# Performance work log

Hardware: AMD Instinct MI355X
Metric: run time of the kernel (lower is better)

Reference implementation:

```python
import jax, jax.numpy as jnp
import numpy as np
from jax import lax

SD = 16          # sample_duration
STRIDE = 16      # feat_stride
SCALES = (4, 8, 16)
RATIOS = (0.5, 1.0, 2.0)
PRE_NMS = 1000   # proposals kept before NMS (TEST config)
POST_NMS = 128   # proposals kept after NMS
NMS_TH = 0.7


def _anchors2d():
    base = 16.0
    ctr = (base - 1.0) / 2.0
    out = []
    for r in RATIOS:
        ws = np.round(np.sqrt(base * base / r))
        hs = np.round(ws * r)
        for s in SCALES:
            w, h = ws * s, hs * s
            out.append([ctr - (w - 1) / 2, ctr - (h - 1) / 2,
                        ctr + (w - 1) / 2, ctr + (h - 1) / 2])
    return np.asarray(out, np.float32)                       # (9, 4)


def _anchors3d():
    # tube anchors: (x1, y1, t1, x2, y2, t2), durations [SD, SD/2, SD/4]
    a2 = _anchors2d()
    out = []
    for d in (SD, SD // 2, SD // 4):
        for a in a2:
            out.append([a[0], a[1], 0.0, a[2], a[3], d - 1.0])
    return np.asarray(out, np.float32)                       # (27, 6)


def _shifted(anchors, H, W):
    k = anchors.shape[-1]
    sx = jnp.arange(W, dtype=jnp.float32) * STRIDE
    sy = jnp.arange(H, dtype=jnp.float32) * STRIDE
    if k == 4:
        sh = jnp.stack(jnp.broadcast_arrays(sx[None, :], sy[:, None],
                                            sx[None, :], sy[:, None]), -1)
    else:
        z = jnp.zeros((H, W), jnp.float32)
        sh = jnp.stack(jnp.broadcast_arrays(sx[None, :], sy[:, None], z,
                                            sx[None, :], sy[:, None], z), -1)
    return (sh[:, :, None, :] + jnp.asarray(anchors)[None, None]).reshape(-1, k)


def _decode(anchors, deltas):
    # deltas layout: (d_ctr..., d_logsize...); works for 2D (k=4) and 3D (k=6)
    nd = anchors.shape[-1] // 2
    lo, hi = anchors[..., :nd], anchors[..., nd:]
    size = hi - lo + 1.0
    ctr = lo + 0.5 * (size - 1.0)
    pctr = deltas[..., :nd] * size + ctr
    psize = jnp.exp(deltas[..., nd:]) * size
    return jnp.concatenate([pctr - 0.5 * (psize - 1.0),
                            pctr + 0.5 * (psize - 1.0)], -1)


def _iou(b, boxes):
    # b: (k,), boxes: (N, k); area/volume IoU with +1 pixel convention
    nd = boxes.shape[-1] // 2
    lo = jnp.maximum(b[:nd], boxes[:, :nd])
    hi = jnp.minimum(b[nd:], boxes[:, nd:])
    inter = jnp.prod(jnp.maximum(hi - lo + 1.0, 0.0), -1)
    va = jnp.prod(b[nd:] - b[:nd] + 1.0)
    vb = jnp.prod(boxes[:, nd:] - boxes[:, :nd] + 1.0, -1)
    return inter / (va + vb - inter)


def _nms(boxes):
    # boxes already sorted by descending score; greedy NMS, fixed output size
    N = boxes.shape[0]

    def body(i, c):
        supp, keep = c
        idx = jnp.argmax(~supp)                 # first unsuppressed box
        keep = keep.at[i].set(idx.astype(jnp.int32))
        supp = supp | (_iou(boxes[idx], boxes) > NMS_TH)
        supp = supp.at[idx].set(True)
        return supp, keep

    _, keep = lax.fori_loop(0, POST_NMS, body,
                            (jnp.zeros(N, bool), jnp.zeros(POST_NMS, jnp.int32)))
    return keep


def _proposals(scores, deltas, anchors, maxs):
    # scores (B,N), deltas (B,N,k), anchors (N,k), maxs (B,1,k)
    boxes = jnp.clip(_decode(anchors[None], deltas), 0.0, maxs)
    _, idx = lax.top_k(scores, PRE_NMS)
    bx = jnp.take_along_axis(boxes, idx[..., None], axis=1)   # (B,PRE,k)
    keep = jax.vmap(_nms)(bx)                                 # (B,POST)
    sel = jnp.take_along_axis(bx, keep[..., None], axis=1)    # (B,POST,k)
    bidx = jnp.broadcast_to(
        jnp.arange(sel.shape[0], dtype=sel.dtype)[:, None, None],
        sel.shape[:2] + (1,))
    return lax.stop_gradient(jnp.concatenate([bidx, sel], -1))


def setup_inputs() -> dict:
    k = jax.random.split(jax.random.key(0), 8)
    s = 0.01
    return {
        "base_feat": jax.random.normal(k[0], (1, 256, 16, 32, 32), jnp.float32),
        "im_info": jnp.array([[512.0, 512.0, 1.0]], jnp.float32),
        "gt_boxes": jax.random.uniform(k[1], (1, 5, 7), jnp.float32) * 100.0,
        "gt_rois": jax.random.uniform(k[2], (1, 5, 16, 5), jnp.float32) * 100.0,
        "W_conv": jax.random.normal(k[3], (512, 256, 3, 3, 3), jnp.float32) * s,
        "b_conv": jnp.zeros((512,), jnp.float32),
        "W_cls": jax.random.normal(k[4], (54, 512), jnp.float32) * s,
        "b_cls": jnp.zeros((54,), jnp.float32),
        "W_bbox": jax.random.normal(k[5], (162, 512), jnp.float32) * s,
        "b_bbox": jnp.zeros((162,), jnp.float32),
        "W_cls16": jax.random.normal(k[6], (18, 512), jnp.float32) * s,
        "b_cls16": jnp.zeros((18,), jnp.float32),
        "W_bbox16": jax.random.normal(k[7], (36, 512), jnp.float32) * s,
        "b_bbox16": jnp.zeros((36,), jnp.float32),
    }


def reference(base_feat, im_info, gt_boxes, gt_rois, W_conv, b_conv,
              W_cls, b_cls, W_bbox, b_bbox, W_cls16, b_cls16,
              W_bbox16, b_bbox16):
    B, _, T, H, W = base_feat.shape
    # RPN_Conv: 3x3x3 Conv3d + ReLU
    conv1 = jax.nn.relu(
        lax.conv_general_dilated(base_feat, W_conv, (1, 1, 1), "SAME",
                                 dimension_numbers=("NCDHW", "OIDHW", "NCDHW"))
        + b_conv[None, :, None, None, None])
    # 1x1x1 score / bbox heads (3D)
    cls3 = jnp.einsum("bcthw,oc->bothw", conv1, W_cls) + b_cls[None, :, None, None, None]
    bbox3 = jnp.einsum("bcthw,oc->bothw", conv1, W_bbox) + b_bbox[None, :, None, None, None]
    # permute(0,1,3,4,2).mean(4) == mean over the temporal axis
    feat2 = conv1.mean(axis=2)
    cls2 = jnp.einsum("bchw,oc->bohw", feat2, W_cls16) + b_cls16[None, :, None, None]
    bbox2 = jnp.einsum("bchw,oc->bohw", feat2, W_bbox16) + b_bbox16[None, :, None, None]
    # reshape(x,2) + softmax over dim 1; fg prob is the second half of channels
    fg3 = jax.nn.softmax(cls3.reshape(B, 2, 27, T, H, W), axis=1)[:, 1]  # (B,27,T,H,W)
    fg2 = jax.nn.softmax(cls2.reshape(B, 2, 9, H, W), axis=1)[:, 1]      # (B,9,H,W)
    # proposal layers consume detached tensors (torch .data)
    fg3, fg2, bbox3d, bbox2d = map(lax.stop_gradient, (fg3, fg2, bbox3, bbox2))
    # flatten position-major (h, w, anchor)
    sc3 = fg3.mean(axis=2).transpose(0, 2, 3, 1).reshape(B, -1)
    dl3 = bbox3d.mean(axis=2).reshape(B, 27, 6, H, W).transpose(0, 3, 4, 1, 2).reshape(B, -1, 6)
    sc2 = fg2.transpose(0, 2, 3, 1).reshape(B, -1)
    dl2 = bbox2d.reshape(B, 9, 4, H, W).transpose(0, 3, 4, 1, 2).reshape(B, -1, 4)
    imh, imw = im_info[:, 0][:, None], im_info[:, 1][:, None]
    sdm = jnp.full_like(imw, SD - 1.0)
    max3 = jnp.stack([imw - 1, imh - 1, sdm, imw - 1, imh - 1, sdm], -1)  # (B,1,6)
    max2 = jnp.stack([imw - 1, imh - 1, imw - 1, imh - 1], -1)            # (B,1,4)
    rois = _proposals(sc3, dl3, _shifted(_anchors3d(), H, W), max3)       # (B,POST,7)
    rois16 = _proposals(sc2, dl2, _shifted(_anchors2d(), H, W), max2)     # (B,POST,5)
    z = jnp.zeros((), jnp.float32)  # eval mode: all RPN losses are 0
    return rois, rois16, z, z, z, z
```

## Files before the change

kernel.cpp:

```cpp
#include <hip/hip_runtime.h>
#include <hip/hip_bf16.h>
#include <cfloat>
#include <cstdint>


#define T_DIM 16
#define H_DIM 32
#define W_DIM 32
#define NVOX  (T_DIM*H_DIM*W_DIM)
#define HW    (H_DIM*W_DIM)
#define CIN   256
#define COUT  512
#define PRE_NMS 1000
#define POST_NMS 128
#define NMS_TH 0.7f

typedef __attribute__((ext_vector_type(8))) short v8s;
typedef __attribute__((ext_vector_type(4))) float v4f;
typedef __attribute__((ext_vector_type(4))) int v4i;

#define MFMA_B16(A,B,C) __builtin_amdgcn_mfma_f32_16x16x32_bf16(A,B,C,0,0,0)

__device__ __forceinline__ short f2bf(float x) {
    unsigned u = __float_as_uint(x);
    u += 0x7FFFu + ((u >> 16) & 1u);
    return (short)(u >> 16);
}
__device__ __forceinline__ float bf2f(short s) {
    return __uint_as_float(((unsigned)(unsigned short)s) << 16);
}
__device__ __forceinline__ int pk(short a, short b) {
    return (int)((unsigned short)a | ((unsigned)(unsigned short)b << 16));
}

__constant__ float c_ws[3] = {23.f, 16.f, 11.f};
__constant__ float c_hs[3] = {12.f, 16.f, 22.f};
__constant__ float c_sc[3] = {4.f, 8.f, 16.f};
__constant__ float c_depth[3] = {16.f, 8.f, 4.f};

__global__ void k_split_w(const float* __restrict__ W, short* __restrict__ A0,
                          short* __restrict__ A1, short* __restrict__ A2) {
    int i = blockIdx.x * 256 + threadIdx.x;
    int c7 = i & 7;
    int o = (i >> 3) & 511;
    int ko = (i >> 12) & 31;
    int tap = i >> 17;
    int c = ko * 8 + c7;
    float x = W[(o * 256 + c) * 27 + tap];
    short h = f2bf(x); float r = x - bf2f(h);
    short m = f2bf(r); float r2 = r - bf2f(m);
    short l = f2bf(r2);
    A0[i] = h; A1[i] = m; A2[i] = l;
}

__global__ void k_build_wcomb(const float* __restrict__ Wcls, const float* __restrict__ Wbb,
                              float* __restrict__ Wc) {
    int i = blockIdx.x * 256 + threadIdx.x;
    int o = i & 255;
    int c = i >> 8;
    float v = 0.f;
    if (o < 54) v = Wcls[o * 512 + c];
    else if (o < 216) v = Wbb[(o - 54) * 512 + c];
    Wc[i] = v;
}

#define SP8(X0,X1,X2,X3,X4,X5,X6,X7, OH, OM, OL) {                            \
    short h0_=f2bf(X0), h1_=f2bf(X1), h2_=f2bf(X2), h3_=f2bf(X3);             \
    short h4_=f2bf(X4), h5_=f2bf(X5), h6_=f2bf(X6), h7_=f2bf(X7);             \
    float r0_=(X0)-bf2f(h0_), r1_=(X1)-bf2f(h1_), r2_=(X2)-bf2f(h2_);         \
    float r3_=(X3)-bf2f(h3_), r4_=(X4)-bf2f(h4_), r5_=(X5)-bf2f(h5_);         \
    float r6_=(X6)-bf2f(h6_), r7_=(X7)-bf2f(h7_);                             \
    short m0_=f2bf(r0_), m1_=f2bf(r1_), m2_=f2bf(r2_), m3_=f2bf(r3_);         \
    short m4_=f2bf(r4_), m5_=f2bf(r5_), m6_=f2bf(r6_), m7_=f2bf(r7_);         \
    short l0_=f2bf(r0_-bf2f(m0_)), l1_=f2bf(r1_-bf2f(m1_));                   \
    short l2_=f2bf(r2_-bf2f(m2_)), l3_=f2bf(r3_-bf2f(m3_));                   \
    short l4_=f2bf(r4_-bf2f(m4_)), l5_=f2bf(r5_-bf2f(m5_));                   \
    short l6_=f2bf(r6_-bf2f(m6_)), l7_=f2bf(r7_-bf2f(m7_));                   \
    OH = (v4i){pk(h0_,h1_), pk(h2_,h3_), pk(h4_,h5_), pk(h6_,h7_)};           \
    OM = (v4i){pk(m0_,m1_), pk(m2_,m3_), pk(m4_,m5_), pk(m6_,m7_)};           \
    OL = (v4i){pk(l0_,l1_), pk(l2_,l3_), pk(l4_,l5_), pk(l6_,l7_)};           \
}

#define CV_SHIFT(TAP) {                                                       \
    int kt_ = (TAP) / 9 - 1, kh_ = ((TAP) / 3) % 3 - 1, kw_ = (TAP) % 3 - 1;  \
    int tt_ = bt + kt_, hh_ = bh + kh_, ww_ = bw + kw_;                       \
    bVal = ((unsigned)tt_ < 16u) && ((unsigned)hh_ < 32u) && ((unsigned)ww_ < 32u); \
    bOff = bVal ? ((tt_ << 10) + (hh_ << 5) + ww_) : 0;                       \
}

#define CV_LOAD_B(CK) {                                                       \
    const float* ip_ = I + ((size_t)((CK) + skh * 16) << 14) + bOff;          \
    float x0_  = bVal ? ip_[0]        : 0.f;                                  \
    float x1_  = bVal ? ip_[1 << 14]  : 0.f;                                  \
    float x2_  = bVal ? ip_[2 << 14]  : 0.f;                                  \
    float x3_  = bVal ? ip_[3 << 14]  : 0.f;                                  \
    float x4_  = bVal ? ip_[4 << 14]  : 0.f;                                  \
    float x5_  = bVal ? ip_[5 << 14]  : 0.f;                                  \
    float x6_  = bVal ? ip_[6 << 14]  : 0.f;                                  \
    float x7_  = bVal ? ip_[7 << 14]  : 0.f;                                  \
    float x8_  = bVal ? ip_[8 << 14]  : 0.f;                                  \
    float x9_  = bVal ? ip_[9 << 14]  : 0.f;                                  \
    float x10_ = bVal ? ip_[10 << 14] : 0.f;                                  \
    float x11_ = bVal ? ip_[11 << 14] : 0.f;                                  \
    float x12_ = bVal ? ip_[12 << 14] : 0.f;                                  \
    float x13_ = bVal ? ip_[13 << 14] : 0.f;                                  \
    float x14_ = bVal ? ip_[14 << 14] : 0.f;                                  \
    float x15_ = bVal ? ip_[15 << 14] : 0.f;                                  \
    SP8(x0_,x1_,x2_,x3_,x4_,x5_,x6_,x7_,       pbh0, pbm0, pbl0);             \
    SP8(x8_,x9_,x10_,x11_,x12_,x13_,x14_,x15_, pbh1, pbm1, pbl1);             \
}

__global__ __launch_bounds__(256) void k_conv3d_mfma(
        const float* __restrict__ I, const short* __restrict__ A0,
        const short* __restrict__ A1, const short* __restrict__ A2,
        const float* __restrict__ bias, float* __restrict__ O) {
    __shared__ v4i Bsh[3][512];
    const int tid = threadIdx.x;
    const int o0 = blockIdx.y * 128;
    const int v0 = blockIdx.x * 128;
    const int lane = tid & 63;
    const int wv = tid >> 6;
    const int quad = lane >> 4, m16 = lane & 15;
    const int wo = (wv >> 1) * 64;
    const int wvx = (wv & 1) * 64;

    const int sa_o = tid >> 1, skh = tid & 1;
    const int uW0 = (skh * 2) * 128 + sa_o;
    const int uW1 = (skh * 2 + 1) * 128 + sa_o;

    const int vbase = v0 + sa_o;
    const int bt = vbase >> 10, bh = (vbase >> 5) & 31, bw = vbase & 31;

    const int uB = quad * 128 + wvx + m16;

    const size_t aLane = ((size_t)(o0 + wo + m16) << 3) + ((size_t)quad << 12);

    v4f acc[4][4];
#pragma unroll
    for (int i = 0; i < 4; i++)
#pragma unroll
        for (int j = 0; j < 4; j++) acc[i][j] = (v4f){0.f, 0.f, 0.f, 0.f};

    int bOff, bVal;
    v4i pbh0, pbh1, pbm0, pbm1, pbl0, pbl1;

    CV_SHIFT(0);
    CV_LOAD_B(0);

    for (int s = 0; s < 216; ++s) {
        __syncthreads();
        Bsh[0][uW0] = pbh0; Bsh[0][uW1] = pbh1;
        Bsh[1][uW0] = pbm0; Bsh[1][uW1] = pbm1;
        Bsh[2][uW0] = pbl0; Bsh[2][uW1] = pbl1;
        __syncthreads();
        const int tap = s >> 3;
        const size_t aBase = (((size_t)tap * 32 + ((s & 7) << 2)) << 12) + aLane;
        v8s ah0 = *(const v8s*)(A0 + aBase);
        v8s ah1 = *(const v8s*)(A0 + aBase + 16 * 8);
        v8s ah2 = *(const v8s*)(A0 + aBase + 32 * 8);
        v8s ah3 = *(const v8s*)(A0 + aBase + 48 * 8);
        v8s am0 = *(const v8s*)(A1 + aBase);
        v8s am1 = *(const v8s*)(A1 + aBase + 16 * 8);
        v8s am2 = *(const v8s*)(A1 + aBase + 32 * 8);
        v8s am3 = *(const v8s*)(A1 + aBase + 48 * 8);
        v8s al0 = *(const v8s*)(A2 + aBase);
        v8s al1 = *(const v8s*)(A2 + aBase + 16 * 8);
        v8s al2 = *(const v8s*)(A2 + aBase + 32 * 8);
        v8s al3 = *(const v8s*)(A2 + aBase + 48 * 8);
        {
            int s1 = s + 1;
            if (s1 < 216) {
                int tap1 = s1 >> 3, ck1 = (s1 & 7) << 5;
                if ((s1 & 7) == 0) CV_SHIFT(tap1);
                CV_LOAD_B(ck1);
            }
        }
#pragma unroll
        for (int j = 0; j < 4; ++j) {
            v8s bb = *(const v8s*)(&Bsh[0][uB + j * 16]);
            v8s bm = *(const v8s*)(&Bsh[1][uB + j * 16]);
            v8s bl = *(const v8s*)(&Bsh[2][uB + j * 16]);
            v4f a;
            a = acc[0][j];
            a = MFMA_B16(ah0, bb, a); a = MFMA_B16(ah0, bm, a);
            a = MFMA_B16(am0, bb, a); a = MFMA_B16(ah0, bl, a);
            a = MFMA_B16(am0, bm, a); a = MFMA_B16(al0, bb, a);
            acc[0][j] = a;
            a = acc[1][j];
            a = MFMA_B16(ah1, bb, a); a = MFMA_B16(ah1, bm, a);
            a = MFMA_B16(am1, bb, a); a = MFMA_B16(ah1, bl, a);
            a = MFMA_B16(am1, bm, a); a = MFMA_B16(al1, bb, a);
            acc[1][j] = a;
            a = acc[2][j];
            a = MFMA_B16(ah2, bb, a); a = MFMA_B16(ah2, bm, a);
            a = MFMA_B16(am2, bb, a); a = MFMA_B16(ah2, bl, a);
            a = MFMA_B16(am2, bm, a); a = MFMA_B16(al2, bb, a);
            acc[2][j] = a;
            a = acc[3][j];
            a = MFMA_B16(ah3, bb, a); a = MFMA_B16(ah3, bm, a);
            a = MFMA_B16(am3, bb, a); a = MFMA_B16(ah3, bl, a);
            a = MFMA_B16(am3, bm, a); a = MFMA_B16(al3, bb, a);
            acc[3][j] = a;
        }
    }

#pragma unroll
    for (int i = 0; i < 4; ++i) {
#pragma unroll
        for (int r = 0; r < 4; ++r) {
            int o = o0 + wo + i * 16 + quad * 4 + r;
            float bo = bias[o];
            float* dst = O + (size_t)o * NVOX + v0 + wvx + m16;
#pragma unroll
            for (int j = 0; j < 4; ++j)
                dst[j * 16] = fmaxf(acc[i][j][r] + bo, 0.f);
        }
    }
}

__global__ __launch_bounds__(256) void k_gemm_logits3(const float* __restrict__ conv1,
                                                      const float* __restrict__ Wc,
                                                      float* __restrict__ L) {
    __shared__ float As[16][128];
    __shared__ float Bs[16][128];
    const int tid = threadIdx.x;
    const int o0 = blockIdx.y * 128;
    const int v0 = blockIdx.x * 128;
    const int ty = tid >> 4, tx = tid & 15;

    float acc[8][8];
#pragma unroll
    for (int i = 0; i < 8; i++)
#pragma unroll
        for (int j = 0; j < 8; j++) acc[i][j] = 0.f;

    for (int ck = 0; ck < 512; ck += 16) {
        __syncthreads();
#pragma unroll
        for (int r = 0; r < 2; ++r) {
            int f = tid + r * 256;
            int c_l = f >> 5, o4 = (f & 31) << 2;
            *(float4*)(&As[c_l][o4]) = *(const float4*)(Wc + ((size_t)(ck + c_l) << 8) + o0 + o4);
        }
#pragma unroll
        for (int r = 0; r < 2; ++r) {
            int f = tid + r * 256;
            int c_l = f >> 5, v4 = (f & 31) << 2;
            *(float4*)(&Bs[c_l][v4]) = *(const float4*)(conv1 + ((size_t)(ck + c_l) << 14) + v0 + v4);
        }
        __syncthreads();
#pragma unroll
        for (int k = 0; k < 16; ++k) {
            float a[8], b[8];
            *(float4*)(a)     = *(const float4*)(&As[k][ty * 4]);
            *(float4*)(a + 4) = *(const float4*)(&As[k][64 + ty * 4]);
            *(float4*)(b)     = *(const float4*)(&Bs[k][tx * 4]);
            *(float4*)(b + 4) = *(const float4*)(&Bs[k][64 + tx * 4]);
#pragma unroll
            for (int i = 0; i < 8; i++)
#pragma unroll
                for (int j = 0; j < 8; j++)
                    acc[i][j] = fmaf(a[i], b[j], acc[i][j]);
        }
    }
#pragma unroll
    for (int i = 0; i < 8; i++) {
        int orow = (i < 4) ? (ty * 4 + i) : (64 + ty * 4 + (i - 4));
        float* dst = L + (size_t)(o0 + orow) * NVOX + v0;
        *(float4*)(dst + tx * 4)      = *(const float4*)(&acc[i][0]);
        *(float4*)(dst + 64 + tx * 4) = *(const float4*)(&acc[i][4]);
    }
}

__global__ void k_sc3(const float* __restrict__ L, const float* __restrict__ b_cls,
                      float* __restrict__ sc3) {
    int i = blockIdx.x * 256 + threadIdx.x;
    if (i >= 27 * HW) return;
    int a = i >> 10, hw = i & 1023;
    float b0 = b_cls[a], b1 = b_cls[27 + a];
    const float* L0 = L + (size_t)a * NVOX + hw;
    const float* L1 = L + (size_t)(27 + a) * NVOX + hw;
    float s = 0.f;
    for (int t = 0; t < T_DIM; t++) {
        float x0 = L0[t * HW] + b0, x1 = L1[t * HW] + b1;
        float m = fmaxf(x0, x1);
        float e0 = expf(x0 - m), e1 = expf(x1 - m);
        s += e1 / (e0 + e1);
    }
    sc3[hw * 27 + a] = s * (1.f / 16.f);
}

__global__ void k_dl3(const float* __restrict__ L, const float* __restrict__ b_bbox,
                      float* __restrict__ dl3) {
    int i = blockIdx.x * 256 + threadIdx.x;
    if (i >= 162 * HW) return;
    int ch = i >> 10, hw = i & 1023;
    const float* Lr = L + (size_t)(54 + ch) * NVOX + hw;
    float s = 0.f;
    for (int t = 0; t < T_DIM; t++) s += Lr[t * HW];
    s = s * (1.f / 16.f) + b_bbox[ch];
    int a = ch / 6, d = ch - a * 6;
    dl3[((size_t)hw * 27 + a) * 6 + d] = s;
}

__global__ void k_feat2(const float* __restrict__ conv1, float* __restrict__ feat2) {
    int i = blockIdx.x * 256 + threadIdx.x;
    int c = i >> 10, hw = i & 1023;
    const float* src = conv1 + (size_t)c * NVOX + hw;
    float s = 0.f;
    for (int t = 0; t < T_DIM; t++) s += src[t * HW];
    feat2[i] = s * (1.f / 16.f);
}

__global__ void k_gemm2d(const float* __restrict__ feat2, const float* __restrict__ Wcls16,
                         const float* __restrict__ Wbb16, float* __restrict__ L2) {
    int g = blockIdx.x * 256 + threadIdx.x;
    int o = g >> 10, hw = g & 1023;
    const float* wrow = (o < 18) ? (Wcls16 + (size_t)o * 512) : (Wbb16 + (size_t)(o - 18) * 512);
    float s = 0.f;
    for (int c = 0; c < 512; c++) s = fmaf(wrow[c], feat2[(size_t)c * HW + hw], s);
    L2[(size_t)o * HW + hw] = s;
}

__global__ void k_sc2(const float* __restrict__ L2, const float* __restrict__ b_cls16,
                      float* __restrict__ sc2) {
    int i = blockIdx.x * 256 + threadIdx.x;
    if (i >= 9 * HW) return;
    int a = i >> 10, hw = i & 1023;
    float x0 = L2[(size_t)a * HW + hw] + b_cls16[a];
    float x1 = L2[(size_t)(9 + a) * HW + hw] + b_cls16[9 + a];
    float m = fmaxf(x0, x1);
    float e0 = expf(x0 - m), e1 = expf(x1 - m);
    sc2[hw * 9 + a] = e1 / (e0 + e1);
}

__global__ void k_dl2(const float* __restrict__ L2, const float* __restrict__ b_bbox16,
                      float* __restrict__ dl2) {
    int i = blockIdx.x * 256 + threadIdx.x;
    if (i >= 36 * HW) return;
    int ch = i >> 10, hw = i & 1023;
    float v = L2[(size_t)(18 + ch) * HW + hw] + b_bbox16[ch];
    int a = ch >> 2, d = ch & 3;
    dl2[((size_t)hw * 9 + a) * 4 + d] = v;
}

__device__ __forceinline__ unsigned mapf(float f) {
    unsigned u = __float_as_uint(f);
    return (u & 0x80000000u) ? ~u : (u | 0x80000000u);
}

__global__ __launch_bounds__(1024) void k_proposal(const float* __restrict__ im_info,
                                                   const float* __restrict__ sc3,
                                                   const float* __restrict__ dl3,
                                                   const float* __restrict__ sc2,
                                                   const float* __restrict__ dl2,
                                                   float* __restrict__ out) {
    const int branch = blockIdx.x;
    const int tid = threadIdx.x;
    const int A = (branch == 0) ? 27 : 9;
    const int nd = (branch == 0) ? 3 : 2;
    const float* scores = (branch == 0) ? sc3 : sc2;
    const float* deltas = (branch == 0) ? dl3 : dl2;
    const int K = PRE_NMS;
    const int ept = A;
    const int base = tid * ept;

    __shared__ unsigned hist[256];
    __shared__ unsigned long long keys[1024];
    __shared__ float bx[PRE_NMS][6];
    __shared__ int keep[POST_NMS];
    __shared__ unsigned wsum[16];
    __shared__ unsigned long long alive[16];
    __shared__ int sh_b, sh_next, bcast;

    unsigned prefix = 0;
    int rank = K;
    for (int shift = 24; shift >= 0; shift -= 8) {
        if (tid < 256) hist[tid] = 0;
        __syncthreads();
        const unsigned mask_hi = (shift == 24) ? 0u : (0xFFFFFFFFu << (shift + 8));
        for (int j = 0; j < ept; j++) {
            unsigned m = mapf(scores[base + j]);
            if ((m & mask_hi) == prefix)
                atomicAdd(&hist[(m >> shift) & 255], 1u);
        }
        __syncthreads();
        for (int d = 1; d < 256; d <<= 1) {
            unsigned add = 0;
            if (tid < 256 && tid + d < 256) add = hist[tid + d];
            __syncthreads();
            if (tid < 256) hist[tid] += add;
            __syncthreads();
        }
        if (tid < 256) {
            bool win = (hist[tid] >= (unsigned)rank) &&
                       (tid == 255 || hist[tid + 1] < (unsigned)rank);
            if (win) { sh_b = tid; sh_next = (tid == 255) ? 0 : (int)hist[tid + 1]; }
        }
        __syncthreads();
        prefix |= (unsigned)sh_b << shift;
        rank -= sh_next;
        __syncthreads();
    }
    const unsigned tau = prefix;

    int gt_c = 0, eq_c = 0;
    for (int j = 0; j < ept; j++) {
        unsigned m = mapf(scores[base + j]);
        gt_c += (m > tau);
        eq_c += (m == tau);
    }
    unsigned cnt = ((unsigned)gt_c << 16) | (unsigned)eq_c;
    const int lane = tid & 63, wid = tid >> 6;
    unsigned x = cnt;
    for (int d = 1; d < 64; d <<= 1) {
        unsigned y = __shfl_up(x, d);
        if (lane >= d) x += y;
    }
    if (lane == 63) wsum[wid] = x;
    __syncthreads();
    if (wid == 0) {
        unsigned w = (lane < 16) ? wsum[lane] : 0;
        for (int d = 1; d < 16; d <<= 1) {
            unsigned y = __shfl_up(w, d);
            if (lane >= d) w += y;
        }
        if (lane < 16) wsum[lane] = w;
    }
    __syncthreads();
    unsigned excl = x - cnt + (wid ? wsum[wid - 1] : 0);
    const int c1 = (int)(wsum[15] >> 16);
    int gi = (int)(excl >> 16);
    int ei = (int)(excl & 0xFFFFu);
    for (int j = 0; j < ept; j++) {
        int idx = base + j;
        unsigned m = mapf(scores[idx]);
        unsigned long long key = ((unsigned long long)m << 32) |
                                 (unsigned)(0xFFFFFFFFu - (unsigned)idx);
        if (m > tau) {
            keys[gi++] = key;
        } else if (m == tau) {
            if (c1 + ei < K) keys[c1 + ei] = key;
            ei++;
        }
    }
    if (tid < 1024 - K) keys[K + tid] = 0;
    __syncthreads();

    for (int k = 2; k <= 1024; k <<= 1) {
        for (int j = k >> 1; j > 0; j >>= 1) {
            int ixj = tid ^ j;
            if (ixj > tid) {
                unsigned long long a = keys[tid], b = keys[ixj];
                bool sw2 = ((tid & k) == 0) ? (a < b) : (a > b);
                if (sw2) { keys[tid] = b; keys[ixj] = a; }
            }
            __syncthreads();
        }
    }

    const float imh = im_info[0], imw = im_info[1];
    if (tid < K) {
        int n = (int)(0xFFFFFFFFu - (unsigned)(keys[tid] & 0xFFFFFFFFull));
        int cell = n / A, a = n - cell * A;
        int hc = cell >> 5, wc = cell & 31;
        int a2 = (branch == 0) ? (a % 9) : a;
        int ri = a2 / 3, si = a2 % 3;
        float w = c_ws[ri] * c_sc[si], h = c_hs[ri] * c_sc[si];
        float lo[3], hi[3], mx[3];
        lo[0] = 7.5f - (w - 1.f) * 0.5f + 16.f * wc;
        hi[0] = 7.5f + (w - 1.f) * 0.5f + 16.f * wc;
        mx[0] = imw - 1.f;
        lo[1] = 7.5f - (h - 1.f) * 0.5f + 16.f * hc;
        hi[1] = 7.5f + (h - 1.f) * 0.5f + 16.f * hc;
        mx[1] = imh - 1.f;
        if (branch == 0) { lo[2] = 0.f; hi[2] = c_depth[a / 9] - 1.f; mx[2] = (float)(T_DIM - 1); }
        const float* dp = deltas + (size_t)n * (2 * nd);
        for (int d = 0; d < nd; d++) {
            float size = hi[d] - lo[d] + 1.f;
            float ctr = lo[d] + 0.5f * (size - 1.f);
            float pctr = dp[d] * size + ctr;
            float psize = expf(dp[nd + d]) * size;
            float pl = pctr - 0.5f * (psize - 1.f);
            float ph = pctr + 0.5f * (psize - 1.f);
            bx[tid][d]      = fminf(fmaxf(pl, 0.f), mx[d]);
            bx[tid][nd + d] = fminf(fmaxf(ph, 0.f), mx[d]);
        }
    }
    if (tid < 16) alive[tid] = (tid < 15) ? ~0ull : ((1ull << (K - 15 * 64)) - 1);
    __syncthreads();

    float myb[6]; float myvol = 1.f;
    if (tid < K) {
        for (int d = 0; d < 6; d++) myb[d] = bx[tid][d];
        for (int d = 0; d < nd; d++) myvol *= (myb[nd + d] - myb[d] + 1.f);
    }
    for (int i = 0; i < POST_NMS; ++i) {
        if (tid < 64) {
            unsigned long long wvb = (tid < 16) ? alive[tid] : 0ull;
            int cand = wvb ? (tid * 64 + __ffsll(wvb) - 1) : 0x7fffffff;
#pragma unroll
            for (int off = 32; off; off >>= 1)
                cand = min(cand, __shfl_xor(cand, off));
            if (tid == 0) {
                int m = (cand == 0x7fffffff) ? 0 : cand;
                bcast = m; keep[i] = m;
            }
        }
        __syncthreads();
        int sel = bcast;
        bool s = false;
        if (tid < K) {
            float inter = 1.f, selvol = 1.f;
            for (int d = 0; d < nd; d++) {
                float slo = bx[sel][d], shi = bx[sel][nd + d];
                float l = fmaxf(slo, myb[d]);
                float hh = fminf(shi, myb[nd + d]);
                inter *= fmaxf(hh - l + 1.f, 0.f);
                selvol *= (shi - slo + 1.f);
            }
            float iou = inter / (selvol + myvol - inter);
            s = (iou > NMS_TH) || (tid == sel);
        }
        unsigned long long bal = __ballot(s);
        if (lane == 0 && bal) alive[wid] &= ~bal;
        __syncthreads();
    }

    if (tid < POST_NMS) {
        int k = keep[tid];
        if (branch == 0) {
            float* o = out + (size_t)tid * 7;
            o[0] = 0.f;
            for (int d = 0; d < 6; d++) o[1 + d] = bx[k][d];
        } else {
            float* o = out + 128 * 7 + (size_t)tid * 5;
            o[0] = 0.f;
            for (int d = 0; d < 4; d++) o[1 + d] = bx[k][d];
        }
    }
    if (branch == 0 && tid == 0) {
        out[1536] = 0.f; out[1537] = 0.f; out[1538] = 0.f; out[1539] = 0.f;
    }
}

extern "C" void kernel_launch(void* const* d_in, const int* in_sizes, int n_in,
                              void* d_out, int out_size, void* d_ws, size_t ws_size,
                              hipStream_t stream) {
    (void)in_sizes; (void)n_in; (void)out_size; (void)ws_size;
    const float* base_feat = (const float*)d_in[0];
    const float* im_info   = (const float*)d_in[1];
    const float* W_conv    = (const float*)d_in[4];
    const float* b_conv    = (const float*)d_in[5];
    const float* W_cls     = (const float*)d_in[6];
    const float* b_cls     = (const float*)d_in[7];
    const float* W_bbox    = (const float*)d_in[8];
    const float* b_bbox    = (const float*)d_in[9];
    const float* W_cls16   = (const float*)d_in[10];
    const float* b_cls16   = (const float*)d_in[11];
    const float* W_bbox16  = (const float*)d_in[12];
    const float* b_bbox16  = (const float*)d_in[13];
    float* out = (float*)d_out;

    char* ws = (char*)d_ws;
    const size_t AW = (size_t)27 * 512 * 256;
    short* A0 = (short*)ws;
    short* A1 = A0 + AW;
    short* A2 = A1 + AW;
    float* L3 = (float*)ws;
    size_t off = AW * 3 * sizeof(short);
    float* Wcomb  = (float*)(ws + off); off += (size_t)512 * 256 * 4;
    float* conv1  = (float*)(ws + off); off += (size_t)COUT * NVOX * 4;
    float* feat2  = (float*)(ws + off); off += (size_t)512 * HW * 4;
    float* L2     = (float*)(ws + off); off += (size_t)64 * HW * 4;
    float* sc3    = (float*)(ws + off); off += (size_t)27 * HW * 4;
    float* dl3    = (float*)(ws + off); off += (size_t)27 * HW * 6 * 4;
    float* sc2    = (float*)(ws + off); off += (size_t)9 * HW * 4;
    float* dl2    = (float*)(ws + off); off += (size_t)9 * HW * 4 * 4;

    k_split_w<<<13824, 256, 0, stream>>>(W_conv, A0, A1, A2);
    k_build_wcomb<<<512, 256, 0, stream>>>(W_cls, W_bbox, Wcomb);
    {
        dim3 g(NVOX / 128, COUT / 128);
        k_conv3d_mfma<<<g, 256, 0, stream>>>(base_feat, A0, A1, A2, b_conv, conv1);
    }
    {
        dim3 g(NVOX / 128, 2);
        k_gemm_logits3<<<g, 256, 0, stream>>>(conv1, Wcomb, L3);
    }
    k_sc3<<<(27 * HW + 255) / 256, 256, 0, stream>>>(L3, b_cls, sc3);
    k_dl3<<<(162 * HW + 255) / 256, 256, 0, stream>>>(L3, b_bbox, dl3);
    k_feat2<<<(512 * HW) / 256, 256, 0, stream>>>(conv1, feat2);
    k_gemm2d<<<(54 * HW) / 256, 256, 0, stream>>>(feat2, W_cls16, W_bbox16, L2);
    k_sc2<<<(9 * HW + 255) / 256, 256, 0, stream>>>(L2, b_cls16, sc2);
    k_dl2<<<(36 * HW + 255) / 256, 256, 0, stream>>>(L2, b_bbox16, dl2);
    k_proposal<<<2, 1024, 0, stream>>>(im_info, sc3, dl3, sc2, dl2, out);
}
```

Before: 983.3 us.

## Double-buffer conv weight fragments and use truncation-based bf16 split

The conv3d MFMA loop now prefetches the next step's A (weight) fragments into a second register set while computing the current step, using a manually unrolled two-stage ping-pong, so global load latency overlaps with MFMA work. The fp32-to-three-bf16 split of the input tile switches from round-to-nearest conversions to bit truncation with byte-permute packing, which cuts ALU work per element. The truncated split still represents the value exactly as a sum of the three parts for typical values, but it raises register pressure because of the doubled A fragment set.

New measurement: 1.274 ms. 29.5% more time.

```diff
diff --git a/kernel.cpp b/kernel.cpp
--- a/kernel.cpp
+++ b/kernel.cpp
@@ -28,9 +28,6 @@
 }
 __device__ __forceinline__ float bf2f(short s) {
     return __uint_as_float(((unsigned)(unsigned short)s) << 16);
-}
-__device__ __forceinline__ int pk(short a, short b) {
-    return (int)((unsigned short)a | ((unsigned)(unsigned short)b << 16));
 }
 
 __constant__ float c_ws[3] = {23.f, 16.f, 11.f};
@@ -64,21 +61,19 @@
     Wc[i] = v;
 }
 
-#define SP8(X0,X1,X2,X3,X4,X5,X6,X7, OH, OM, OL) {                            \
-    short h0_=f2bf(X0), h1_=f2bf(X1), h2_=f2bf(X2), h3_=f2bf(X3);             \
-    short h4_=f2bf(X4), h5_=f2bf(X5), h6_=f2bf(X6), h7_=f2bf(X7);             \
-    float r0_=(X0)-bf2f(h0_), r1_=(X1)-bf2f(h1_), r2_=(X2)-bf2f(h2_);         \
-    float r3_=(X3)-bf2f(h3_), r4_=(X4)-bf2f(h4_), r5_=(X5)-bf2f(h5_);         \
-    float r6_=(X6)-bf2f(h6_), r7_=(X7)-bf2f(h7_);                             \
-    short m0_=f2bf(r0_), m1_=f2bf(r1_), m2_=f2bf(r2_), m3_=f2bf(r3_);         \
-    short m4_=f2bf(r4_), m5_=f2bf(r5_), m6_=f2bf(r6_), m7_=f2bf(r7_);         \
-    short l0_=f2bf(r0_-bf2f(m0_)), l1_=f2bf(r1_-bf2f(m1_));                   \
-    short l2_=f2bf(r2_-bf2f(m2_)), l3_=f2bf(r3_-bf2f(m3_));                   \
-    short l4_=f2bf(r4_-bf2f(m4_)), l5_=f2bf(r5_-bf2f(m5_));                   \
-    short l6_=f2bf(r6_-bf2f(m6_)), l7_=f2bf(r7_-bf2f(m7_));                   \
-    OH = (v4i){pk(h0_,h1_), pk(h2_,h3_), pk(h4_,h5_), pk(h6_,h7_)};           \
-    OM = (v4i){pk(m0_,m1_), pk(m2_,m3_), pk(m4_,m5_), pk(m6_,m7_)};           \
-    OL = (v4i){pk(l0_,l1_), pk(l2_,l3_), pk(l4_,l5_), pk(l6_,l7_)};           \
+#define SPLIT2(X0, X1, OH, OM, OL) {                                          \
+    unsigned u0_ = __float_as_uint(X0), u1_ = __float_as_uint(X1);            \
+    OH = (int)__builtin_amdgcn_perm(u1_, u0_, 0x07060302u);                   \
+    float h0_ = __uint_as_float(u0_ & 0xFFFF0000u);                           \
+    float h1_ = __uint_as_float(u1_ & 0xFFFF0000u);                           \
+    float r0_ = (X0) - h0_, r1_ = (X1) - h1_;                                 \
+    unsigned v0_ = __float_as_uint(r0_), v1_ = __float_as_uint(r1_);          \
+    OM = (int)__builtin_amdgcn_perm(v1_, v0_, 0x07060302u);                   \
+    float m0_ = __uint_as_float(v0_ & 0xFFFF0000u);                           \
+    float m1_ = __uint_as_float(v1_ & 0xFFFF0000u);                           \
+    float s0_ = r0_ - m0_, s1_ = r1_ - m1_;                                   \
+    OL = (int)__builtin_amdgcn_perm(__float_as_uint(s1_),                     \
+                                    __float_as_uint(s0_), 0x07060302u);       \
 }
 
 #define CV_SHIFT(TAP) {                                                       \
@@ -106,8 +101,81 @@
     float x13_ = bVal ? ip_[13 << 14] : 0.f;                                  \
     float x14_ = bVal ? ip_[14 << 14] : 0.f;                                  \
     float x15_ = bVal ? ip_[15 << 14] : 0.f;                                  \
-    SP8(x0_,x1_,x2_,x3_,x4_,x5_,x6_,x7_,       pbh0, pbm0, pbl0);             \
-    SP8(x8_,x9_,x10_,x11_,x12_,x13_,x14_,x15_, pbh1, pbm1, pbl1);             \
+    int h01,h23,h45,h67,m01,m23,m45,m67,l01,l23,l45,l67;                      \
+    SPLIT2(x0_,  x1_,  h01, m01, l01);                                        \
+    SPLIT2(x2_,  x3_,  h23, m23, l23);                                        \
+    SPLIT2(x4_,  x5_,  h45, m45, l45);                                        \
+    SPLIT2(x6_,  x7_,  h67, m67, l67);                                        \
+    pbh0 = (v4i){h01, h23, h45, h67};                                         \
+    pbm0 = (v4i){m01, m23, m45, m67};                                         \
+    pbl0 = (v4i){l01, l23, l45, l67};                                         \
+    SPLIT2(x8_,  x9_,  h01, m01, l01);                                        \
+    SPLIT2(x10_, x11_, h23, m23, l23);                                        \
+    SPLIT2(x12_, x13_, h45, m45, l45);                                        \
+    SPLIT2(x14_, x15_, h67, m67, l67);                                        \
+    pbh1 = (v4i){h01, h23, h45, h67};                                         \
+    pbm1 = (v4i){m01, m23, m45, m67};                                         \
+    pbl1 = (v4i){l01, l23, l45, l67};                                         \
+}
+
+#define DECL_ASET(P) v8s P##h0, P##h1, P##h2, P##h3, P##m0, P##m1, P##m2,     \
+                         P##m3, P##l0, P##l1, P##l2, P##l3;
+
+#define LOAD_ASET(P, S) {                                                     \
+    const size_t aB_ = (((size_t)((S) >> 3) * 32 + (((S) & 7) << 2)) << 12) + aLane; \
+    P##h0 = *(const v8s*)(A0 + aB_);       P##h1 = *(const v8s*)(A0 + aB_ + 128); \
+    P##h2 = *(const v8s*)(A0 + aB_ + 256); P##h3 = *(const v8s*)(A0 + aB_ + 384); \
+    P##m0 = *(const v8s*)(A1 + aB_);       P##m1 = *(const v8s*)(A1 + aB_ + 128); \
+    P##m2 = *(const v8s*)(A1 + aB_ + 256); P##m3 = *(const v8s*)(A1 + aB_ + 384); \
+    P##l0 = *(const v8s*)(A2 + aB_);       P##l1 = *(const v8s*)(A2 + aB_ + 128); \
+    P##l2 = *(const v8s*)(A2 + aB_ + 256); P##l3 = *(const v8s*)(A2 + aB_ + 384); \
+}
+
+#define COMPUTE(P) {                                                          \
+    _Pragma("unroll")                                                         \
+    for (int j = 0; j < 4; ++j) {                                             \
+        v8s bb = *(const v8s*)(&Bsh[0][uB + j * 16]);                         \
+        v8s bm = *(const v8s*)(&Bsh[1][uB + j * 16]);                         \
+        v8s bl = *(const v8s*)(&Bsh[2][uB + j * 16]);                         \
+        v4f a;                                                                \
+        a = acc[0][j];                                                        \
+        a = MFMA_B16(P##h0, bb, a); a = MFMA_B16(P##h0, bm, a);               \
+        a = MFMA_B16(P##m0, bb, a); a = MFMA_B16(P##h0, bl, a);               \
+        a = MFMA_B16(P##m0, bm, a); a = MFMA_B16(P##l0, bb, a);               \
+        acc[0][j] = a;                                                        \
+        a = acc[1][j];                                                        \
+        a = MFMA_B16(P##h1, bb, a); a = MFMA_B16(P##h1, bm, a);               \
+        a = MFMA_B16(P##m1, bb, a); a = MFMA_B16(P##h1, bl, a);               \
+        a = MFMA_B16(P##m1, bm, a); a = MFMA_B16(P##l1, bb, a);               \
+        acc[1][j] = a;                                                        \
+        a = acc[2][j];                                                        \
+        a = MFMA_B16(P##h2, bb, a); a = MFMA_B16(P##h2, bm, a);               \
+        a = MFMA_B16(P##m2, bb, a); a = MFMA_B16(P##h2, bl, a);               \
+        a = MFMA_B16(P##m2, bm, a); a = MFMA_B16(P##l2, bb, a);               \
+        acc[2][j] = a;                                                        \
+        a = acc[3][j];                                                        \
+        a = MFMA_B16(P##h3, bb, a); a = MFMA_B16(P##h3, bm, a);               \
+        a = MFMA_B16(P##m3, bb, a); a = MFMA_B16(P##h3, bl, a);               \
+        a = MFMA_B16(P##m3, bm, a); a = MFMA_B16(P##l3, bb, a);               \
+        acc[3][j] = a;                                                        \
+    }                                                                         \
+}
+
+#define CONV_STAGE(S, CUR, NXT) {                                             \
+    __syncthreads();                                                          \
+    Bsh[0][uW0] = pbh0; Bsh[0][uW1] = pbh1;                                   \
+    Bsh[1][uW0] = pbm0; Bsh[1][uW1] = pbm1;                                   \
+    Bsh[2][uW0] = pbl0; Bsh[2][uW1] = pbl1;                                   \
+    __syncthreads();                                                          \
+    {                                                                         \
+        int s1_ = (S) + 1;                                                    \
+        if (s1_ < 216) {                                                      \
+            LOAD_ASET(NXT, s1_);                                              \
+            if ((s1_ & 7) == 0) CV_SHIFT(s1_ >> 3);                           \
+            CV_LOAD_B((s1_ & 7) << 5);                                        \
+        }                                                                     \
+    }                                                                         \
+    COMPUTE(CUR);                                                             \
 }
 
 __global__ __launch_bounds__(256) void k_conv3d_mfma(
@@ -143,65 +211,16 @@
 
     int bOff, bVal;
     v4i pbh0, pbh1, pbm0, pbm1, pbl0, pbl1;
+    DECL_ASET(wA);
+    DECL_ASET(wB);
 
     CV_SHIFT(0);
     CV_LOAD_B(0);
-
-    for (int s = 0; s < 216; ++s) {
-        __syncthreads();
-        Bsh[0][uW0] = pbh0; Bsh[0][uW1] = pbh1;
-        Bsh[1][uW0] = pbm0; Bsh[1][uW1] = pbm1;
-        Bsh[2][uW0] = pbl0; Bsh[2][uW1] = pbl1;
-        __syncthreads();
-        const int tap = s >> 3;
-        const size_t aBase = (((size_t)tap * 32 + ((s & 7) << 2)) << 12) + aLane;
-        v8s ah0 = *(const v8s*)(A0 + aBase);
-        v8s ah1 = *(const v8s*)(A0 + aBase + 16 * 8);
-        v8s ah2 = *(const v8s*)(A0 + aBase + 32 * 8);
-        v8s ah3 = *(const v8s*)(A0 + aBase + 48 * 8);
-        v8s am0 = *(const v8s*)(A1 + aBase);
-        v8s am1 = *(const v8s*)(A1 + aBase + 16 * 8);
-        v8s am2 = *(const v8s*)(A1 + aBase + 32 * 8);
-        v8s am3 = *(const v8s*)(A1 + aBase + 48 * 8);
-        v8s al0 = *(const v8s*)(A2 + aBase);
-        v8s al1 = *(const v8s*)(A2 + aBase + 16 * 8);
-        v8s al2 = *(const v8s*)(A2 + aBase + 32 * 8);
-        v8s al3 = *(const v8s*)(A2 + aBase + 48 * 8);
-        {
-            int s1 = s + 1;
-            if (s1 < 216) {
-                int tap1 = s1 >> 3, ck1 = (s1 & 7) << 5;
-                if ((s1 & 7) == 0) CV_SHIFT(tap1);
-                CV_LOAD_B(ck1);
-            }
-        }
-#pragma unroll
-        for (int j = 0; j < 4; ++j) {
-            v8s bb = *(const v8s*)(&Bsh[0][uB + j * 16]);
-            v8s bm = *(const v8s*)(&Bsh[1][uB + j * 16]);
-            v8s bl = *(const v8s*)(&Bsh[2][uB + j * 16]);
-            v4f a;
-            a = acc[0][j];
-            a = MFMA_B16(ah0, bb, a); a = MFMA_B16(ah0, bm, a);
-            a = MFMA_B16(am0, bb, a); a = MFMA_B16(ah0, bl, a);
-            a = MFMA_B16(am0, bm, a); a = MFMA_B16(al0, bb, a);
-            acc[0][j] = a;
-            a = acc[1][j];
-            a = MFMA_B16(ah1, bb, a); a = MFMA_B16(ah1, bm, a);
-            a = MFMA_B16(am1, bb, a); a = MFMA_B16(ah1, bl, a);
-            a = MFMA_B16(am1, bm, a); a = MFMA_B16(al1, bb, a);
-            acc[1][j] = a;
-            a = acc[2][j];
-            a = MFMA_B16(ah2, bb, a); a = MFMA_B16(ah2, bm, a);
-            a = MFMA_B16(am2, bb, a); a = MFMA_B16(ah2, bl, a);
-            a = MFMA_B16(am2, bm, a); a = MFMA_B16(al2, bb, a);
-            acc[2][j] = a;
-            a = acc[3][j];
-            a = MFMA_B16(ah3, bb, a); a = MFMA_B16(ah3, bm, a);
-            a = MFMA_B16(am3, bb, a); a = MFMA_B16(ah3, bl, a);
-            a = MFMA_B16(am3, bm, a); a = MFMA_B16(al3, bb, a);
-            acc[3][j] = a;
-        }
+    LOAD_ASET(wA, 0);
+
+    for (int s = 0; s < 216; s += 2) {
+        CONV_STAGE(s,     wA, wB);
+        CONV_STAGE(s + 1, wB, wA);
     }
 
 #pragma unroll
```
